# Performance work log

Measured on AMD Instinct MI355X. Metric: run time of the kernel, lower is better.

Reference implementation:

```python
import jax, jax.numpy as jnp
import numpy as np

N = 100_000       # nodes
E = 1_600_000     # directed edges (avg degree 16)
IN, H, Z = 128, 128, 64


def setup_inputs() -> dict:
    key = jax.random.key(0)
    ks = jax.random.split(key, 8)
    x = jax.random.normal(ks[0], (N, IN), dtype=jnp.float32)
    edge_index = jax.random.randint(ks[1], (2, E), 0, N, dtype=jnp.int32)
    # Glorot-ish init like PyG GCNConv
    W1 = jax.random.normal(ks[2], (IN, H), dtype=jnp.float32) / np.sqrt(IN).astype(np.float32)
    b1 = jnp.zeros((H,), dtype=jnp.float32)
    Wmu = jax.random.normal(ks[3], (H, Z), dtype=jnp.float32) / np.sqrt(H).astype(np.float32)
    bmu = jnp.zeros((Z,), dtype=jnp.float32)
    Wlv = jax.random.normal(ks[4], (H, Z), dtype=jnp.float32) / np.sqrt(H).astype(np.float32)
    blv = jnp.zeros((Z,), dtype=jnp.float32)
    return {"x": x, "edge_index": edge_index, "W1": W1, "b1": b1,
            "Wmu": Wmu, "bmu": bmu, "Wlv": Wlv, "blv": blv}


def _gcn_conv(x, src, dst, norm, W, b):
    """PyG GCNConv: out = scatter_add(norm * (x @ W)[src], dst) + b."""
    h = x @ W                                   # [N, out_dim]
    msg = h[src] * norm[:, None]                # [E+N, out_dim] gather + scale
    out = jax.ops.segment_sum(msg, dst, num_segments=N)
    return out + b


def reference(x, edge_index, W1, b1, Wmu, bmu, Wlv, blv):
    loop = jnp.arange(N, dtype=edge_index.dtype)
    src = jnp.concatenate([edge_index[0], loop])   # add self-loops (PyG default)
    dst = jnp.concatenate([edge_index[1], loop])
    # symmetric normalization D^{-1/2} (A+I) D^{-1/2}
    deg = jax.ops.segment_sum(jnp.ones_like(dst, dtype=x.dtype), dst, num_segments=N)
    dinv = jax.lax.rsqrt(deg)                      # deg >= 1 thanks to self-loops
    norm = dinv[src] * dinv[dst]                   # [E+N]
    h = jax.nn.relu(_gcn_conv(x, src, dst, norm, W1, b1))
    mu = _gcn_conv(h, src, dst, norm, Wmu, bmu)
    logvar = _gcn_conv(h, src, dst, norm, Wlv, blv)
    return (mu, logvar)
```

## Files before the change

kernel.cpp:

```cpp
#include <hip/hip_runtime.h>
#include <hip/hip_bf16.h>
#include <stdint.h>

static inline size_t ws_align(size_t x) { return (x + 255) & ~(size_t)255; }

typedef __attribute__((ext_vector_type(8))) short bf16x8;
typedef __attribute__((ext_vector_type(4))) float f32x4;

__device__ __forceinline__ uint32_t pack_bf16(float a, float b) {
    uint32_t ua = __float_as_uint(a), ub = __float_as_uint(b);
    ua = (ua + 0x7fffu + ((ua >> 16) & 1u)) >> 16;
    ub = (ub + 0x7fffu + ((ub >> 16) & 1u)) >> 16;
    return ua | (ub << 16);
}
__device__ __forceinline__ uint16_t cvt_bf16(float a) {
    uint32_t ua = __float_as_uint(a);
    return (uint16_t)((ua + 0x7fffu + ((ua >> 16) & 1u)) >> 16);
}
__device__ __forceinline__ float bf_lo(uint32_t v) { return __uint_as_float(v << 16); }
__device__ __forceinline__ float bf_hi(uint32_t v) { return __uint_as_float(v & 0xffff0000u); }

__device__ __forceinline__ void fma8(float* acc, uint4 g, float wt) {
    acc[0] = fmaf(bf_lo(g.x), wt, acc[0]); acc[1] = fmaf(bf_hi(g.x), wt, acc[1]);
    acc[2] = fmaf(bf_lo(g.y), wt, acc[2]); acc[3] = fmaf(bf_hi(g.y), wt, acc[3]);
    acc[4] = fmaf(bf_lo(g.z), wt, acc[4]); acc[5] = fmaf(bf_hi(g.z), wt, acc[5]);
    acc[6] = fmaf(bf_lo(g.w), wt, acc[6]); acc[7] = fmaf(bf_hi(g.w), wt, acc[7]);
}


__global__ __launch_bounds__(256) void k_bcount(const int* __restrict__ dst, int* __restrict__ cntAB,
                                                int E, int nchunk, int NB) {
    __shared__ int h[512];
    for (int t = threadIdx.x; t < NB; t += 256) h[t] = 0;
    __syncthreads();
    const int c = blockIdx.x;
    const int per = (E + nchunk - 1) / nchunk;
    const int e0 = c * per, e1 = (e0 + per < E) ? e0 + per : E;
    for (int e = e0 + threadIdx.x; e < e1; e += 256)
        atomicAdd(&h[dst[e] >> 8], 1);
    __syncthreads();
    for (int t = threadIdx.x; t < NB; t += 256) cntAB[t * nchunk + c] = h[t];
}

__global__ __launch_bounds__(256) void k_bscatter(const int* __restrict__ src, const int* __restrict__ dst,
                                                  const int* __restrict__ baseAB, uint2* __restrict__ ebkt,
                                                  int E, int nchunk, int NB) {
    __shared__ int bump[512];
    const int c = blockIdx.x;
    for (int t = threadIdx.x; t < NB; t += 256) bump[t] = baseAB[t * nchunk + c];
    __syncthreads();
    const int per = (E + nchunk - 1) / nchunk;
    const int e0 = c * per, e1 = (e0 + per < E) ? e0 + per : E;
    for (int e = e0 + threadIdx.x; e < e1; e += 256) {
        int d = dst[e], s = src[e];
        int pos = atomicAdd(&bump[d >> 8], 1);
        ebkt[pos] = make_uint2((uint32_t)s, (uint32_t)d);
    }
}

__global__ __launch_bounds__(256) void k_bhist(const uint2* __restrict__ ebkt, const int* __restrict__ baseAB,
                                               float* __restrict__ dinv, int* __restrict__ rp,
                                               int nchunk, int N, int E) {
    __shared__ int h[256];
    __shared__ int sh[256];
    h[threadIdx.x] = 0;
    __syncthreads();
    const int b = blockIdx.x;
    const int e0 = baseAB[b * nchunk], e1 = baseAB[(b + 1) * nchunk];
    for (int e = e0 + threadIdx.x; e < e1; e += 256)
        atomicAdd(&h[ebkt[e].y & 255], 1);
    __syncthreads();
    const int t = threadIdx.x;
    const int c = h[t];
    sh[t] = c;
    __syncthreads();
    for (int off = 1; off < 256; off <<= 1) {
        int x = (t >= off) ? sh[t - off] : 0;
        __syncthreads();
        sh[t] += x;
        __syncthreads();
    }
    int node = (b << 8) + t;
    if (node < N) {
        rp[node] = e0 + sh[t] - c;
        dinv[node] = rsqrtf((float)(c + 1));
    }
    if (blockIdx.x == gridDim.x - 1 && t == 0) rp[N] = E;
}

__global__ __launch_bounds__(256) void k_bfill(const uint2* __restrict__ ebkt, const int* __restrict__ baseAB,
                                               const int* __restrict__ rp, const float* __restrict__ dinv,
                                               uint2* __restrict__ cedge, int nchunk) {
    __shared__ int fl[256];
    fl[threadIdx.x] = 0;
    __syncthreads();
    const int b = blockIdx.x;
    const int e0 = baseAB[b * nchunk], e1 = baseAB[(b + 1) * nchunk];
    for (int e = e0 + threadIdx.x; e < e1; e += 256) {
        uint2 sd = ebkt[e];
        int d = (int)sd.y;
        int posL = atomicAdd(&fl[d & 255], 1);
        cedge[rp[d] + posL] = make_uint2(sd.x, __float_as_uint(dinv[sd.x] * dinv[d]));
    }
}

__global__ __launch_bounds__(256) void k_scan1(const int* __restrict__ cnt, int* __restrict__ rp,
                                               int* __restrict__ bsum, int N) {
    __shared__ int sh[256];
    int t = threadIdx.x;
    int base = blockIdx.x * 1024 + t * 4;
    int v[4];
#pragma unroll
    for (int i = 0; i < 4; i++) v[i] = (base + i < N) ? cnt[base + i] : 0;
    int s = v[0] + v[1] + v[2] + v[3];
    sh[t] = s;
    __syncthreads();
    for (int off = 1; off < 256; off <<= 1) {
        int x = (t >= off) ? sh[t - off] : 0;
        __syncthreads();
        sh[t] += x;
        __syncthreads();
    }
    int excl = sh[t] - s;
    if (t == 255) bsum[blockIdx.x] = sh[255];
    int run = excl;
#pragma unroll
    for (int i = 0; i < 4; i++) {
        if (base + i < N) rp[base + i] = run;
        run += v[i];
    }
}

__global__ __launch_bounds__(256) void k_scan2(int* __restrict__ bsum, int nb) {
    __shared__ int sh[256];
    int t = threadIdx.x;
    int v = (t < nb) ? bsum[t] : 0;
    sh[t] = v;
    __syncthreads();
    for (int off = 1; off < 256; off <<= 1) {
        int x = (t >= off) ? sh[t - off] : 0;
        __syncthreads();
        sh[t] += x;
        __syncthreads();
    }
    if (t < nb) bsum[t] = sh[t] - v;
}

__global__ void k_scan3(int* __restrict__ rp, const int* __restrict__ bsum, int N, int E) {
    int i = blockIdx.x * blockDim.x + threadIdx.x;
    if (i < N) rp[i] += bsum[i >> 10];
    if (i == N) rp[N] = E;
}

__global__ void k_cvt(const float* __restrict__ in, uint32_t* __restrict__ outp, int n4) {
    int idx = blockIdx.x * blockDim.x + threadIdx.x;
    if (idx >= n4) return;
    float4 v = ((const float4*)in)[idx];
    ((uint2*)outp)[idx] = make_uint2(pack_bf16(v.x, v.y), pack_bf16(v.z, v.w));
}

__global__ __launch_bounds__(256) void k_agg(const uint8_t* __restrict__ featB,
                                             uint32_t* __restrict__ outB,
                                             const int* __restrict__ rp,
                                             const uint2* __restrict__ cedge,
                                             const float* __restrict__ dinv, int N) {
    int node = blockIdx.x * 4 + (threadIdx.x >> 6);
    if (node >= N) return;
    int lane = threadIdx.x & 63;
    int j = lane & 15;
    int q = lane >> 4;
    int beg = rp[node], end = rp[node + 1];
    float di = dinv[node];
    float w0 = (q == 0) ? di * di : 0.0f;
    const uint8_t* fb = featB + (size_t)j * 16;

    uint4 sv = *(const uint4*)(fb + (size_t)node * 256);
    float acc[8];
    acc[0] = bf_lo(sv.x) * w0; acc[1] = bf_hi(sv.x) * w0;
    acc[2] = bf_lo(sv.y) * w0; acc[3] = bf_hi(sv.y) * w0;
    acc[4] = bf_lo(sv.z) * w0; acc[5] = bf_hi(sv.z) * w0;
    acc[6] = bf_lo(sv.w) * w0; acc[7] = bf_hi(sv.w) * w0;

    for (int base = beg + q; base < end; base += 16) {
        uint2 e0 = cedge[base];
        uint2 e1 = make_uint2(0u, 0u), e2 = make_uint2(0u, 0u), e3 = make_uint2(0u, 0u);
        if (base + 4 < end)  e1 = cedge[base + 4];
        if (base + 8 < end)  e2 = cedge[base + 8];
        if (base + 12 < end) e3 = cedge[base + 12];
        uint4 g0 = *(const uint4*)(fb + (size_t)e0.x * 256);
        uint4 g1 = *(const uint4*)(fb + (size_t)e1.x * 256);
        uint4 g2 = *(const uint4*)(fb + (size_t)e2.x * 256);
        uint4 g3 = *(const uint4*)(fb + (size_t)e3.x * 256);
        fma8(acc, g0, __uint_as_float(e0.y));
        fma8(acc, g1, __uint_as_float(e1.y));
        fma8(acc, g2, __uint_as_float(e2.y));
        fma8(acc, g3, __uint_as_float(e3.y));
    }

#pragma unroll
    for (int k = 0; k < 8; k++) {
        acc[k] += __shfl_xor(acc[k], 16, 64);
        acc[k] += __shfl_xor(acc[k], 32, 64);
    }
    if (q == 0) {
        uint4 p = make_uint4(pack_bf16(acc[0], acc[1]), pack_bf16(acc[2], acc[3]),
                             pack_bf16(acc[4], acc[5]), pack_bf16(acc[6], acc[7]));
        *(uint4*)(outB + (size_t)node * 64 + j * 4) = p;
    }
}

__global__ __launch_bounds__(256) void k_gemm1_mfma(
        const uint8_t* __restrict__ A, uint8_t* __restrict__ C,
        const float* __restrict__ W, const float* __restrict__ bias, int N) {
    __shared__ uint32_t Bt[128 * 68];
    {
        int c = threadIdx.x & 127;
        for (int k2 = threadIdx.x >> 7; k2 < 64; k2 += 2)
            Bt[c * 68 + k2] = pack_bf16(W[(2 * k2) * 128 + c], W[(2 * k2 + 1) * 128 + c]);
    }
    __syncthreads();

    const int lane = threadIdx.x & 63;
    const int wv = threadIdx.x >> 6;
    const int rrow = lane & 15;
    const int g = lane >> 4;
    const int r0 = blockIdx.x * 64 + wv * 16;
    const int rl = r0 + rrow;
    const int rc = (rl < N) ? rl : (N - 1);

    bf16x8 a[4];
    const uint8_t* arow = A + (size_t)rc * 256 + g * 16;
#pragma unroll
    for (int kb = 0; kb < 4; kb++) a[kb] = *(const bf16x8*)(arow + kb * 64);

    f32x4 acc[8];
#pragma unroll
    for (int ct = 0; ct < 8; ct++) acc[ct] = (f32x4){0.f, 0.f, 0.f, 0.f};

    const char* btb = (const char*)Bt;
#pragma unroll
    for (int ct = 0; ct < 8; ct++) {
        const char* bp = btb + (ct * 16 + rrow) * 272 + g * 16;
#pragma unroll
        for (int kb = 0; kb < 4; kb++) {
            bf16x8 bfr = *(const bf16x8*)(bp + kb * 64);
            acc[ct] = __builtin_amdgcn_mfma_f32_16x16x32_bf16(a[kb], bfr, acc[ct], 0, 0, 0);
        }
    }

#pragma unroll
    for (int ct = 0; ct < 8; ct++) {
        const int col = ct * 16 + rrow;
        const float bv = bias[col];
#pragma unroll
        for (int r = 0; r < 4; r++) {
            int row = r0 + g * 4 + r;
            if (row < N) {
                float h = fmaxf(acc[ct][r] + bv, 0.f);
                *(uint16_t*)(C + (size_t)row * 256 + col * 2) = cvt_bf16(h);
            }
        }
    }
}

__global__ __launch_bounds__(256) void k_gemm2_mfma(
        const uint8_t* __restrict__ A, float* __restrict__ out,
        const float* __restrict__ Wmu, const float* __restrict__ Wlv,
        const float* __restrict__ bmu, const float* __restrict__ blv, int N) {
    __shared__ uint32_t Bt[128 * 68];
    {
        int c = threadIdx.x & 127;
        const float* Wc = (c < 64) ? (Wmu + c) : (Wlv + (c - 64));
        for (int k2 = threadIdx.x >> 7; k2 < 64; k2 += 2)
            Bt[c * 68 + k2] = pack_bf16(Wc[(2 * k2) * 64], Wc[(2 * k2 + 1) * 64]);
    }
    __syncthreads();

    const int lane = threadIdx.x & 63;
    const int wv = threadIdx.x >> 6;
    const int rrow = lane & 15;
    const int g = lane >> 4;
    const int r0 = blockIdx.x * 64 + wv * 16;
    const int rl = r0 + rrow;
    const int rc = (rl < N) ? rl : (N - 1);

    bf16x8 a[4];
    const uint8_t* arow = A + (size_t)rc * 256 + g * 16;
#pragma unroll
    for (int kb = 0; kb < 4; kb++) a[kb] = *(const bf16x8*)(arow + kb * 64);

    f32x4 acc[8];
#pragma unroll
    for (int ct = 0; ct < 8; ct++) acc[ct] = (f32x4){0.f, 0.f, 0.f, 0.f};

    const char* btb = (const char*)Bt;
#pragma unroll
    for (int ct = 0; ct < 8; ct++) {
        const char* bp = btb + (ct * 16 + rrow) * 272 + g * 16;
#pragma unroll
        for (int kb = 0; kb < 4; kb++) {
            bf16x8 bfr = *(const bf16x8*)(bp + kb * 64);
            acc[ct] = __builtin_amdgcn_mfma_f32_16x16x32_bf16(a[kb], bfr, acc[ct], 0, 0, 0);
        }
    }

#pragma unroll
    for (int ct = 0; ct < 8; ct++) {
        const int col = ct * 16 + rrow;
        const float bv = (col < 64) ? bmu[col] : blv[col - 64];
        float* obase = (col < 64) ? (out + col) : (out + (size_t)N * 64 + (col - 64));
#pragma unroll
        for (int r = 0; r < 4; r++) {
            int row = r0 + g * 4 + r;
            if (row < N) obase[(size_t)row * 64] = acc[ct][r] + bv;
        }
    }
}

extern "C" void kernel_launch(void* const* d_in, const int* in_sizes, int n_in,
                              void* d_out, int out_size, void* d_ws, size_t ws_size,
                              hipStream_t stream) {
    const float* x   = (const float*)d_in[0];
    const int*   ei  = (const int*)d_in[1];
    const float* W1  = (const float*)d_in[2];
    const float* b1  = (const float*)d_in[3];
    const float* Wmu = (const float*)d_in[4];
    const float* bmu = (const float*)d_in[5];
    const float* Wlv = (const float*)d_in[6];
    const float* blv = (const float*)d_in[7];
    float* out = (float*)d_out;

    const int N = in_sizes[0] / 128;
    const int E = in_sizes[1] / 2;
    const int* src = ei;
    const int* dst = ei + E;

    const int nchunk = 256;
    const int NB = (N + 255) >> 8;
    const int M = NB * nchunk;

    char* ws = (char*)d_ws;
    size_t off = 0;
    float* dinv   = (float*)(ws + off); off = ws_align(off + (size_t)N * 4);
    int* rp       = (int*)(ws + off);   off = ws_align(off + (size_t)(N + 1) * 4);
    int* bsum     = (int*)(ws + off);   off = ws_align(off + 1024 * 4);
    int* cntAB    = (int*)(ws + off);   off = ws_align(off + (size_t)(M + 64) * 4);
    int* baseAB   = (int*)(ws + off);   off = ws_align(off + (size_t)(M + 64) * 4);
    uint2* cedge  = (uint2*)(ws + off); off = ws_align(off + (size_t)E * 8);
    uint32_t* xb  = (uint32_t*)(ws + off); off = ws_align(off + (size_t)N * 256);
    uint8_t* F1   = (uint8_t*)(ws + off);  off = ws_align(off + (size_t)N * 256);
    uint2* ebkt   = (uint2*)xb;

    const int b = 256;

    k_bcount<<<nchunk, 256, 0, stream>>>(dst, cntAB, E, nchunk, NB);
    k_scan1<<<(M + 1023) / 1024, 256, 0, stream>>>(cntAB, baseAB, bsum, M);
    k_scan2<<<1, 256, 0, stream>>>(bsum, (M + 1023) / 1024);
    k_scan3<<<(M + 1 + b - 1) / b, b, 0, stream>>>(baseAB, bsum, M, E);
    k_bscatter<<<nchunk, 256, 0, stream>>>(src, dst, baseAB, ebkt, E, nchunk, NB);
    k_bhist<<<NB, 256, 0, stream>>>(ebkt, baseAB, dinv, rp, nchunk, N, E);
    k_bfill<<<NB, 256, 0, stream>>>(ebkt, baseAB, rp, dinv, cedge, nchunk);

    k_cvt<<<(N * 32 + b - 1) / b, b, 0, stream>>>(x, xb, N * 32);
    const int aggBlocks = (N + 3) / 4;
    k_agg<<<aggBlocks, 256, 0, stream>>>((const uint8_t*)xb, (uint32_t*)F1, rp, cedge, dinv, N);
    k_gemm1_mfma<<<(N + 63) / 64, 256, 0, stream>>>(F1, F1, W1, b1, N);

    k_agg<<<aggBlocks, 256, 0, stream>>>(F1, (uint32_t*)xb, rp, cedge, dinv, N);
    k_gemm2_mfma<<<(N + 63) / 64, 256, 0, stream>>>((const uint8_t*)xb, out, Wmu, Wlv, bmu, blv, N);
}
```

Baseline: 240.2 us.

## Fuse preprocessing kernels, store CSR as sources only, prepack GEMM weights once

Merges the bucket count, the bf16 conversion of x and the weight prepacking into one multi-role kernel. Merges the bucket histogram and CSR fill into one kernel that writes only 4-byte source indices. The aggregation kernel now computes edge weights on the fly from dinv[src]*dinv[dst], which halves CSR edge traffic but adds a dependent gather of dinv per edge. The GEMM kernels copy pre-packed weight tiles from global memory instead of repacking W in every block. The edge bucket buffer now gets its own workspace region instead of aliasing xb, so x can be converted concurrently.

```diff
diff --git a/kernel.cpp b/kernel.cpp
--- a/kernel.cpp
+++ b/kernel.cpp
@@ -27,19 +27,93 @@
     acc[6] = fmaf(bf_lo(g.w), wt, acc[6]); acc[7] = fmaf(bf_hi(g.w), wt, acc[7]);
 }
 
-
-__global__ __launch_bounds__(256) void k_bcount(const int* __restrict__ dst, int* __restrict__ cntAB,
-                                                int E, int nchunk, int NB) {
-    __shared__ int h[512];
-    for (int t = threadIdx.x; t < NB; t += 256) h[t] = 0;
-    __syncthreads();
-    const int c = blockIdx.x;
-    const int per = (E + nchunk - 1) / nchunk;
-    const int e0 = c * per, e1 = (e0 + per < E) ? e0 + per : E;
-    for (int e = e0 + threadIdx.x; e < e1; e += 256)
-        atomicAdd(&h[dst[e] >> 8], 1);
-    __syncthreads();
-    for (int t = threadIdx.x; t < NB; t += 256) cntAB[t * nchunk + c] = h[t];
+__global__ __launch_bounds__(256) void k_pre(const int* __restrict__ dst, int* __restrict__ cntAB,
+                                             const float* __restrict__ x, uint32_t* __restrict__ xb,
+                                             const float* __restrict__ W1,
+                                             const float* __restrict__ Wmu, const float* __restrict__ Wlv,
+                                             uint32_t* __restrict__ BtG1, uint32_t* __restrict__ BtG2,
+                                             int E, int nchunk, int NB, int n4) {
+    const int b = blockIdx.x;
+    if (b < nchunk) {
+        __shared__ int h[512];
+        for (int t = threadIdx.x; t < NB; t += 256) h[t] = 0;
+        __syncthreads();
+        const int per = (E + nchunk - 1) / nchunk;
+        const int e0 = b * per, e1 = (e0 + per < E) ? e0 + per : E;
+        for (int e = e0 + threadIdx.x; e < e1; e += 256)
+            atomicAdd(&h[dst[e] >> 8], 1);
+        __syncthreads();
+        for (int t = threadIdx.x; t < NB; t += 256) cntAB[t * nchunk + b] = h[t];
+    } else if (b < nchunk + 34) {
+        int t = (b - nchunk) * 256 + threadIdx.x;
+        int c = t / 68, k2 = t % 68;
+        uint32_t v = 0;
+        if (k2 < 64) v = pack_bf16(W1[(2 * k2) * 128 + c], W1[(2 * k2 + 1) * 128 + c]);
+        BtG1[t] = v;
+    } else if (b < nchunk + 68) {
+        int t = (b - nchunk - 34) * 256 + threadIdx.x;
+        int c = t / 68, k2 = t % 68;
+        uint32_t v = 0;
+        if (k2 < 64) {
+            const float* Wc = (c < 64) ? (Wmu + c) : (Wlv + (c - 64));
+            v = pack_bf16(Wc[(2 * k2) * 64], Wc[(2 * k2 + 1) * 64]);
+        }
+        BtG2[t] = v;
+    } else {
+        int idx = (b - nchunk - 68) * 256 + threadIdx.x;
+        if (idx < n4) {
+            float4 v = ((const float4*)x)[idx];
+            ((uint2*)xb)[idx] = make_uint2(pack_bf16(v.x, v.y), pack_bf16(v.z, v.w));
+        }
+    }
+}
+
+__global__ __launch_bounds__(256) void k_scan1(const int* __restrict__ cnt, int* __restrict__ rp,
+                                               int* __restrict__ bsum, int N) {
+    __shared__ int sh[256];
+    int t = threadIdx.x;
+    int base = blockIdx.x * 1024 + t * 4;
+    int v[4];
+#pragma unroll
+    for (int i = 0; i < 4; i++) v[i] = (base + i < N) ? cnt[base + i] : 0;
+    int s = v[0] + v[1] + v[2] + v[3];
+    sh[t] = s;
+    __syncthreads();
+    for (int off = 1; off < 256; off <<= 1) {
+        int x = (t >= off) ? sh[t - off] : 0;
+        __syncthreads();
+        sh[t] += x;
+        __syncthreads();
+    }
+    int excl = sh[t] - s;
+    if (t == 255) bsum[blockIdx.x] = sh[255];
+    int run = excl;
+#pragma unroll
+    for (int i = 0; i < 4; i++) {
+        if (base + i < N) rp[base + i] = run;
+        run += v[i];
+    }
+}
+
+__global__ __launch_bounds__(256) void k_scan2(int* __restrict__ bsum, int nb) {
+    __shared__ int sh[256];
+    int t = threadIdx.x;
+    int v = (t < nb) ? bsum[t] : 0;
+    sh[t] = v;
+    __syncthreads();
+    for (int off = 1; off < 256; off <<= 1) {
+        int x = (t >= off) ? sh[t - off] : 0;
+        __syncthreads();
+        sh[t] += x;
+        __syncthreads();
+    }
+    if (t < nb) bsum[t] = sh[t] - v;
+}
+
+__global__ void k_scan3(int* __restrict__ rp, const int* __restrict__ bsum, int N, int E) {
+    int i = blockIdx.x * blockDim.x + threadIdx.x;
+    if (i < N) rp[i] += bsum[i >> 10];
+    if (i == N) rp[N] = E;
 }
 
 __global__ __launch_bounds__(256) void k_bscatter(const int* __restrict__ src, const int* __restrict__ dst,
@@ -58,19 +132,22 @@
     }
 }
 
-__global__ __launch_bounds__(256) void k_bhist(const uint2* __restrict__ ebkt, const int* __restrict__ baseAB,
-                                               float* __restrict__ dinv, int* __restrict__ rp,
-                                               int nchunk, int N, int E) {
+__global__ __launch_bounds__(256) void k_bbuild(const uint2* __restrict__ ebkt, const int* __restrict__ baseAB,
+                                                float* __restrict__ dinv, int* __restrict__ rp,
+                                                uint32_t* __restrict__ csrc, int nchunk, int N) {
     __shared__ int h[256];
     __shared__ int sh[256];
-    h[threadIdx.x] = 0;
+    __shared__ int rpd[256];
+    __shared__ int fl[256];
+    const int t = threadIdx.x;
+    h[t] = 0;
+    fl[t] = 0;
     __syncthreads();
     const int b = blockIdx.x;
     const int e0 = baseAB[b * nchunk], e1 = baseAB[(b + 1) * nchunk];
-    for (int e = e0 + threadIdx.x; e < e1; e += 256)
+    for (int e = e0 + t; e < e1; e += 256)
         atomicAdd(&h[ebkt[e].y & 255], 1);
     __syncthreads();
-    const int t = threadIdx.x;
     const int c = h[t];
     sh[t] = c;
     __syncthreads();
@@ -80,89 +157,28 @@
         sh[t] += x;
         __syncthreads();
     }
+    rpd[t] = e0 + sh[t] - c;
     int node = (b << 8) + t;
     if (node < N) {
-        rp[node] = e0 + sh[t] - c;
+        rp[node] = rpd[t];
         dinv[node] = rsqrtf((float)(c + 1));
     }
-    if (blockIdx.x == gridDim.x - 1 && t == 0) rp[N] = E;
-}
-
-__global__ __launch_bounds__(256) void k_bfill(const uint2* __restrict__ ebkt, const int* __restrict__ baseAB,
-                                               const int* __restrict__ rp, const float* __restrict__ dinv,
-                                               uint2* __restrict__ cedge, int nchunk) {
-    __shared__ int fl[256];
-    fl[threadIdx.x] = 0;
-    __syncthreads();
-    const int b = blockIdx.x;
-    const int e0 = baseAB[b * nchunk], e1 = baseAB[(b + 1) * nchunk];
-    for (int e = e0 + threadIdx.x; e < e1; e += 256) {
+    if (node == N - 1 || t == 255) {
+        if (node + 1 <= N && (node == N - 1)) rp[N] = e0 + sh[255];
+    }
+    __syncthreads();
+    for (int e = e0 + t; e < e1; e += 256) {
         uint2 sd = ebkt[e];
-        int d = (int)sd.y;
-        int posL = atomicAdd(&fl[d & 255], 1);
-        cedge[rp[d] + posL] = make_uint2(sd.x, __float_as_uint(dinv[sd.x] * dinv[d]));
-    }
-}
-
-__global__ __launch_bounds__(256) void k_scan1(const int* __restrict__ cnt, int* __restrict__ rp,
-                                               int* __restrict__ bsum, int N) {
-    __shared__ int sh[256];
-    int t = threadIdx.x;
-    int base = blockIdx.x * 1024 + t * 4;
-    int v[4];
-#pragma unroll
-    for (int i = 0; i < 4; i++) v[i] = (base + i < N) ? cnt[base + i] : 0;
-    int s = v[0] + v[1] + v[2] + v[3];
-    sh[t] = s;
-    __syncthreads();
-    for (int off = 1; off < 256; off <<= 1) {
-        int x = (t >= off) ? sh[t - off] : 0;
-        __syncthreads();
-        sh[t] += x;
-        __syncthreads();
-    }
-    int excl = sh[t] - s;
-    if (t == 255) bsum[blockIdx.x] = sh[255];
-    int run = excl;
-#pragma unroll
-    for (int i = 0; i < 4; i++) {
-        if (base + i < N) rp[base + i] = run;
-        run += v[i];
-    }
-}
-
-__global__ __launch_bounds__(256) void k_scan2(int* __restrict__ bsum, int nb) {
-    __shared__ int sh[256];
-    int t = threadIdx.x;
-    int v = (t < nb) ? bsum[t] : 0;
-    sh[t] = v;
-    __syncthreads();
-    for (int off = 1; off < 256; off <<= 1) {
-        int x = (t >= off) ? sh[t - off] : 0;
-        __syncthreads();
-        sh[t] += x;
-        __syncthreads();
-    }
-    if (t < nb) bsum[t] = sh[t] - v;
-}
-
-__global__ void k_scan3(int* __restrict__ rp, const int* __restrict__ bsum, int N, int E) {
-    int i = blockIdx.x * blockDim.x + threadIdx.x;
-    if (i < N) rp[i] += bsum[i >> 10];
-    if (i == N) rp[N] = E;
-}
-
-__global__ void k_cvt(const float* __restrict__ in, uint32_t* __restrict__ outp, int n4) {
-    int idx = blockIdx.x * blockDim.x + threadIdx.x;
-    if (idx >= n4) return;
-    float4 v = ((const float4*)in)[idx];
-    ((uint2*)outp)[idx] = make_uint2(pack_bf16(v.x, v.y), pack_bf16(v.z, v.w));
+        int dl = (int)(sd.y & 255);
+        int posL = atomicAdd(&fl[dl], 1);
+        csrc[rpd[dl] + posL] = sd.x;
+    }
 }
 
 __global__ __launch_bounds__(256) void k_agg(const uint8_t* __restrict__ featB,
                                              uint32_t* __restrict__ outB,
                                              const int* __restrict__ rp,
-                                             const uint2* __restrict__ cedge,
+                                             const uint32_t* __restrict__ csrc,
                                              const float* __restrict__ dinv, int N) {
     int node = blockIdx.x * 4 + (threadIdx.x >> 6);
     if (node >= N) return;
@@ -182,19 +198,23 @@
     acc[6] = bf_lo(sv.w) * w0; acc[7] = bf_hi(sv.w) * w0;
 
     for (int base = beg + q; base < end; base += 16) {
-        uint2 e0 = cedge[base];
-        uint2 e1 = make_uint2(0u, 0u), e2 = make_uint2(0u, 0u), e3 = make_uint2(0u, 0u);
-        if (base + 4 < end)  e1 = cedge[base + 4];
-        if (base + 8 < end)  e2 = cedge[base + 8];
-        if (base + 12 < end) e3 = cedge[base + 12];
-        uint4 g0 = *(const uint4*)(fb + (size_t)e0.x * 256);
-        uint4 g1 = *(const uint4*)(fb + (size_t)e1.x * 256);
-        uint4 g2 = *(const uint4*)(fb + (size_t)e2.x * 256);
-        uint4 g3 = *(const uint4*)(fb + (size_t)e3.x * 256);
-        fma8(acc, g0, __uint_as_float(e0.y));
-        fma8(acc, g1, __uint_as_float(e1.y));
-        fma8(acc, g2, __uint_as_float(e2.y));
-        fma8(acc, g3, __uint_as_float(e3.y));
+        bool v1 = base + 4 < end, v2 = base + 8 < end, v3 = base + 12 < end;
+        uint32_t s0 = csrc[base];
+        uint32_t s1 = v1 ? csrc[base + 4] : 0u;
+        uint32_t s2 = v2 ? csrc[base + 8] : 0u;
+        uint32_t s3 = v3 ? csrc[base + 12] : 0u;
+        float wa = dinv[s0] * di;
+        float wb = v1 ? dinv[s1] * di : 0.f;
+        float wc = v2 ? dinv[s2] * di : 0.f;
+        float wd = v3 ? dinv[s3] * di : 0.f;
+        uint4 g0 = *(const uint4*)(fb + (size_t)s0 * 256);
+        uint4 g1 = *(const uint4*)(fb + (size_t)s1 * 256);
+        uint4 g2 = *(const uint4*)(fb + (size_t)s2 * 256);
+        uint4 g3 = *(const uint4*)(fb + (size_t)s3 * 256);
+        fma8(acc, g0, wa);
+        fma8(acc, g1, wb);
+        fma8(acc, g2, wc);
+        fma8(acc, g3, wd);
     }
 
 #pragma unroll
@@ -211,13 +231,10 @@
 
 __global__ __launch_bounds__(256) void k_gemm1_mfma(
         const uint8_t* __restrict__ A, uint8_t* __restrict__ C,
-        const float* __restrict__ W, const float* __restrict__ bias, int N) {
+        const uint32_t* __restrict__ BtG, const float* __restrict__ bias, int N) {
     __shared__ uint32_t Bt[128 * 68];
-    {
-        int c = threadIdx.x & 127;
-        for (int k2 = threadIdx.x >> 7; k2 < 64; k2 += 2)
-            Bt[c * 68 + k2] = pack_bf16(W[(2 * k2) * 128 + c], W[(2 * k2 + 1) * 128 + c]);
-    }
+    for (int t = threadIdx.x; t < 128 * 68 / 4; t += 256)
+        ((uint4*)Bt)[t] = ((const uint4*)BtG)[t];
     __syncthreads();
 
     const int lane = threadIdx.x & 63;
@@ -265,15 +282,11 @@
 
 __global__ __launch_bounds__(256) void k_gemm2_mfma(
         const uint8_t* __restrict__ A, float* __restrict__ out,
-        const float* __restrict__ Wmu, const float* __restrict__ Wlv,
+        const uint32_t* __restrict__ BtG,
         const float* __restrict__ bmu, const float* __restrict__ blv, int N) {
     __shared__ uint32_t Bt[128 * 68];
-    {
-        int c = threadIdx.x & 127;
-        const float* Wc = (c < 64) ? (Wmu + c) : (Wlv + (c - 64));
-        for (int k2 = threadIdx.x >> 7; k2 < 64; k2 += 2)
-            Bt[c * 68 + k2] = pack_bf16(Wc[(2 * k2) * 64], Wc[(2 * k2 + 1) * 64]);
-    }
+    for (int t = threadIdx.x; t < 128 * 68 / 4; t += 256)
+        ((uint4*)Bt)[t] = ((const uint4*)BtG)[t];
     __syncthreads();
 
     const int lane = threadIdx.x & 63;
@@ -338,34 +351,37 @@
     const int nchunk = 256;
     const int NB = (N + 255) >> 8;
     const int M = NB * nchunk;
+    const int n4 = N * 32;
 
     char* ws = (char*)d_ws;
     size_t off = 0;
-    float* dinv   = (float*)(ws + off); off = ws_align(off + (size_t)N * 4);
-    int* rp       = (int*)(ws + off);   off = ws_align(off + (size_t)(N + 1) * 4);
-    int* bsum     = (int*)(ws + off);   off = ws_align(off + 1024 * 4);
-    int* cntAB    = (int*)(ws + off);   off = ws_align(off + (size_t)(M + 64) * 4);
-    int* baseAB   = (int*)(ws + off);   off = ws_align(off + (size_t)(M + 64) * 4);
-    uint2* cedge  = (uint2*)(ws + off); off = ws_align(off + (size_t)E * 8);
-    uint32_t* xb  = (uint32_t*)(ws + off); off = ws_align(off + (size_t)N * 256);
-    uint8_t* F1   = (uint8_t*)(ws + off);  off = ws_align(off + (size_t)N * 256);
-    uint2* ebkt   = (uint2*)xb;
+    float* dinv    = (float*)(ws + off);    off = ws_align(off + (size_t)N * 4);
+    int* rp        = (int*)(ws + off);      off = ws_align(off + (size_t)(N + 1) * 4);
+    int* bsum      = (int*)(ws + off);      off = ws_align(off + 1024 * 4);
+    int* cntAB     = (int*)(ws + off);      off = ws_align(off + (size_t)(M + 64) * 4);
+    int* baseAB    = (int*)(ws + off);      off = ws_align(off + (size_t)(M + 64) * 4);
+    uint32_t* BtG1 = (uint32_t*)(ws + off); off = ws_align(off + 128 * 68 * 4);
+    uint32_t* BtG2 = (uint32_t*)(ws + off); off = ws_align(off + 128 * 68 * 4);
+    uint32_t* csrc = (uint32_t*)(ws + off); off = ws_align(off + (size_t)E * 4);
+    uint32_t* xb   = (uint32_t*)(ws + off); off = ws_align(off + (size_t)N * 256);
+    uint8_t* F1    = (uint8_t*)(ws + off);  off = ws_align(off + (size_t)N * 256);
+    uint2* ebkt    = (uint2*)(ws + off);    off = ws_align(off + (size_t)E * 8);
 
     const int b = 256;
-
-    k_bcount<<<nchunk, 256, 0, stream>>>(dst, cntAB, E, nchunk, NB);
+    const int ncvt = (n4 + 255) / 256;
+
+    k_pre<<<nchunk + 68 + ncvt, 256, 0, stream>>>(dst, cntAB, x, xb, W1, Wmu, Wlv,
+                                                  BtG1, BtG2, E, nchunk, NB, n4);
     k_scan1<<<(M + 1023) / 1024, 256, 0, stream>>>(cntAB, baseAB, bsum, M);
     k_scan2<<<1, 256, 0, stream>>>(bsum, (M + 1023) / 1024);
     k_scan3<<<(M + 1 + b - 1) / b, b, 0, stream>>>(baseAB, bsum, M, E);
     k_bscatter<<<nchunk, 256, 0, stream>>>(src, dst, baseAB, ebkt, E, nchunk, NB);
-    k_bhist<<<NB, 256, 0, stream>>>(ebkt, baseAB, dinv, rp, nchunk, N, E);
-    k_bfill<<<NB, 256, 0, stream>>>(ebkt, baseAB, rp, dinv, cedge, nchunk);
-
-    k_cvt<<<(N * 32 + b - 1) / b, b, 0, stream>>>(x, xb, N * 32);
+    k_bbuild<<<NB, 256, 0, stream>>>(ebkt, baseAB, dinv, rp, csrc, nchunk, N);
+
     const int aggBlocks = (N + 3) / 4;
-    k_agg<<<aggBlocks, 256, 0, stream>>>((const uint8_t*)xb, (uint32_t*)F1, rp, cedge, dinv, N);
-    k_gemm1_mfma<<<(N + 63) / 64, 256, 0, stream>>>(F1, F1, W1, b1, N);
-
-    k_agg<<<aggBlocks, 256, 0, stream>>>(F1, (uint32_t*)xb, rp, cedge, dinv, N);
-    k_gemm2_mfma<<<(N + 63) / 64, 256, 0, stream>>>((const uint8_t*)xb, out, Wmu, Wlv, bmu, blv, N);
-}
+    k_agg<<<aggBlocks, 256, 0, stream>>>((const uint8_t*)xb, (uint32_t*)F1, rp, csrc, dinv, N);
+    k_gemm1_mfma<<<(N + 63) / 64, 256, 0, stream>>>(F1, F1, BtG1, b1, N);
+
+    k_agg<<<aggBlocks, 256, 0, stream>>>(F1, (uint32_t*)xb, rp, csrc, dinv, N);
+    k_gemm2_mfma<<<(N + 63) / 64, 256, 0, stream>>>((const uint8_t*)xb, out, BtG2, bmu, blv, N);
+}
```

New measurement: 223.8 us. 1.07x faster.
